# Kernel optimization log

Hardware: AMD Instinct MI355X
Metric: run time of the kernel (lower is better)

## Reference

```python
import jax, jax.numpy as jnp
import numpy as np

MODEL_DIM = 768
NUM_HEADS = 6
HEAD_DIM = 128
T = 4096
EPS = float(jnp.finfo(jnp.float32).eps)


def _rms_norm(x):
    # F.rms_norm(x, (x.size(-1),)) with no weight
    return x * jax.lax.rsqrt(jnp.mean(x * x, axis=-1, keepdims=True) + EPS)


def _rotary_tables(max_len, head_dim):
    # angular_freq: (1/1024)**linspace(0,1,dim//4) then pad dim//4 zeros -> half dim = dim//2
    nf = head_dim // 4
    af = (1.0 / 1024.0) ** jnp.linspace(0.0, 1.0, nf, dtype=jnp.float32)
    af = jnp.concatenate([af, jnp.zeros(nf, dtype=jnp.float32)])  # [head_dim//2]
    t = jnp.arange(max_len, dtype=jnp.float32)
    theta = jnp.einsum('i,j->ij', t, af)  # [max_len, head_dim//2]
    return jnp.cos(theta), jnp.sin(theta)


def _apply_rotary(x_bthd, pos_id, cos_tab, sin_tab):
    cos = cos_tab[pos_id][:, None, :]  # [T,1,hd/2] -> broadcast over heads
    sin = sin_tab[pos_id][:, None, :]
    x1, x2 = jnp.split(x_bthd.astype(jnp.float32), 2, axis=-1)
    y1 = x1 * cos + x2 * sin
    y2 = -x1 * sin + x2 * cos
    return jnp.concatenate([y1, y2], axis=-1).astype(x_bthd.dtype)


def setup_inputs() -> dict:
    key = jax.random.key(0)
    ks = jax.random.split(key, 8)
    bound = (3.0 ** 0.5) * 0.5 * MODEL_DIM ** (-0.5)  # CastedLinear init
    x = jax.random.normal(ks[0], (1, T, MODEL_DIM), dtype=jnp.float32)
    v_residual = jax.random.normal(ks[1], (1, T, NUM_HEADS, HEAD_DIM), dtype=jnp.float32)
    pos_id = jnp.arange(T, dtype=jnp.int32)
    mask = jnp.tril(jnp.ones((T, T), dtype=bool))  # causal block_mask equivalent
    Wq = jax.random.uniform(ks[2], (MODEL_DIM, MODEL_DIM), jnp.float32, -bound, bound)
    Wk = jax.random.uniform(ks[3], (MODEL_DIM, MODEL_DIM), jnp.float32, -bound, bound)
    Wv = jax.random.uniform(ks[4], (MODEL_DIM, MODEL_DIM), jnp.float32, -bound, bound)
    Wo = jax.random.uniform(ks[5], (MODEL_DIM, MODEL_DIM), jnp.float32, -bound, bound)
    lamb = jnp.float32(0.5)
    return {"x": x, "v_residual": v_residual, "Wq": Wq, "Wk": Wk, "Wv": Wv,
            "Wo": Wo, "lamb": lamb, "pos_id": pos_id, "mask": mask}


def reference(x, v_residual, Wq, Wk, Wv, Wo, lamb, pos_id, mask):
    B, Tn, _ = x.shape
    cos_tab, sin_tab = _rotary_tables(Tn, HEAD_DIM)
    # QKV projections (F.linear: x @ W.T)
    q = (x @ Wq.T).reshape(B, Tn, NUM_HEADS, HEAD_DIM)
    k = (x @ Wk.T).reshape(B, Tn, NUM_HEADS, HEAD_DIM)
    v = (x @ Wv.T).reshape(B, Tn, NUM_HEADS, HEAD_DIM)
    q = _apply_rotary(_rms_norm(q), pos_id, cos_tab, sin_tab)
    k = _apply_rotary(_rms_norm(k), pos_id, cos_tab, sin_tab)
    # value-residual mixing
    v = (1.0 - lamb) * v + lamb * v_residual
    # attention with block mask (scale = 1/sqrt(head_dim), flex_attention default)
    scale = 1.0 / (HEAD_DIM ** 0.5)
    scores = jnp.einsum('bthd,bshd->bhts', q, k) * scale  # [B,H,T,T]
    scores = jnp.where(mask[None, None, :, :], scores, -jnp.inf)
    attn = jax.nn.softmax(scores, axis=-1)
    y = jnp.einsum('bhts,bshd->bthd', attn, v).reshape(B, Tn, NUM_HEADS * HEAD_DIM)
    return (y @ Wo.T, v_residual)
```

## Files before the change

### kernel.cpp

```cpp
#include <hip/hip_runtime.h>
#include <hip/hip_bf16.h>

typedef unsigned short u16;
typedef __attribute__((ext_vector_type(8))) short short8;
typedef __attribute__((ext_vector_type(4))) float f32x4;
typedef __attribute__((ext_vector_type(16))) float f32x16;
typedef __attribute__((ext_vector_type(2))) unsigned int u32x2;

#define MODEL 768
#define SCALE2 0.1275174137f

__device__ __forceinline__ float bf2f(u16 u) {
  unsigned int x = ((unsigned int)u) << 16;
  return __uint_as_float(x);
}
__device__ __forceinline__ u16 f2bf(float f) {
  unsigned int x = __float_as_uint(f);
  unsigned int r = (x + 0x7FFFu + ((x >> 16) & 1u)) >> 16;
  return (u16)r;
}
__device__ __forceinline__ void lds_ld16(const u16* g, u16* l) {
  __builtin_amdgcn_global_load_lds((const __attribute__((address_space(1))) void*)g,
                                   (__attribute__((address_space(3))) void*)l, 16, 0, 0);
}
__device__ __forceinline__ unsigned int cvtpk_bf16(float lo, float hi_) {
  unsigned int r;
  asm("v_cvt_pk_bf16_f32 %0, %1, %2" : "=v"(r) : "v"(lo), "v"(hi_));
  return r;
}

__global__ __launch_bounds__(256) void r24_cvt(const float* __restrict__ x,
                                               const float* __restrict__ wq,
                                               const float* __restrict__ wk,
                                               const float* __restrict__ wv,
                                               u16* __restrict__ xb,
                                               u16* __restrict__ wqb,
                                               u16* __restrict__ wkb,
                                               u16* __restrict__ wvb) {
  int i = blockIdx.x * 256 + threadIdx.x;
  const float* src;
  u16* dst;
  int j;
  if (i < 786432) { src = x; dst = xb; j = i; }
  else if (i < 933888) { src = wq; dst = wqb; j = i - 786432; }
  else if (i < 1081344) { src = wk; dst = wkb; j = i - 933888; }
  else { src = wv; dst = wvb; j = i - 1081344; }
  float4 v = ((const float4*)src)[j];
  ushort4 o;
  o.x = f2bf(v.x); o.y = f2bf(v.y); o.z = f2bf(v.z); o.w = f2bf(v.w);
  ((ushort4*)dst)[j] = o;
}

__global__ __launch_bounds__(256) void r24_gemm_qkv(const u16* __restrict__ A,
                                                    const u16* __restrict__ W0,
                                                    const u16* __restrict__ W1,
                                                    const u16* __restrict__ W2,
                                                    u16* __restrict__ C0,
                                                    u16* __restrict__ C1,
                                                    u16* __restrict__ C2) {
  const u16* Wb = (blockIdx.z == 0) ? W0 : (blockIdx.z == 1) ? W1 : W2;
  u16* C = (blockIdx.z == 0) ? C0 : (blockIdx.z == 1) ? C1 : C2;
  __shared__ u16 As[64 * 64];
  __shared__ u16 Bs[128 * 64];
  const int tid = threadIdx.x;
  const int w = tid >> 6, l = tid & 63;
  const int lr = l & 15, lg = l >> 4;
  const int m0 = blockIdx.x * 64, n0 = blockIdx.y * 128;
  const int wr = (w >> 1) * 32, wc = (w & 1) * 64;
  const int srow = l >> 3;
  const int sblk = l & 7;
  f32x4 acc[2][4] = {};
  for (int k0 = 0; k0 < 768; k0 += 64) {
    __syncthreads();
#pragma unroll
    for (int i = 0; i < 2; i++) {
      int ii = w * 2 + i;
      int row = ii * 8 + srow;
      int blk = sblk ^ (row & 7);
      lds_ld16(A + (size_t)(m0 + row) * 768 + k0 + blk * 8, As + ii * 512);
    }
#pragma unroll
    for (int i = 0; i < 4; i++) {
      int ii = w * 4 + i;
      int row = ii * 8 + srow;
      int blk = sblk ^ (row & 7);
      lds_ld16(Wb + (size_t)(n0 + row) * 768 + k0 + blk * 8, Bs + ii * 512);
    }
    __syncthreads();
#pragma unroll
    for (int kk = 0; kk < 2; kk++) {
      short8 af[2], bfr[4];
#pragma unroll
      for (int mr = 0; mr < 2; mr++) {
        int r = wr + mr * 16 + lr;
        af[mr] = *(const short8*)(As + r * 64 + (((kk * 4 + lg) ^ (r & 7)) * 8));
      }
#pragma unroll
      for (int nc = 0; nc < 4; nc++) {
        int r = wc + nc * 16 + lr;
        bfr[nc] = *(const short8*)(Bs + r * 64 + (((kk * 4 + lg) ^ (r & 7)) * 8));
      }
#pragma unroll
      for (int mr = 0; mr < 2; mr++)
#pragma unroll
        for (int nc = 0; nc < 4; nc++)
          acc[mr][nc] = __builtin_amdgcn_mfma_f32_16x16x32_bf16(af[mr], bfr[nc], acc[mr][nc], 0, 0, 0);
    }
  }
#pragma unroll
  for (int mr = 0; mr < 2; mr++)
#pragma unroll
    for (int nc = 0; nc < 4; nc++)
#pragma unroll
      for (int ri = 0; ri < 4; ri++) {
        int row = m0 + wr + mr * 16 + lg * 4 + ri;
        int col = n0 + wc + nc * 16 + lr;
        C[(size_t)row * 768 + col] = f2bf(acc[mr][nc][ri]);
      }
}

__global__ __launch_bounds__(256) void r24_gemm_proj(const float* __restrict__ accO,
                                                     const float* __restrict__ accL,
                                                     const u16* __restrict__ Wb,
                                                     float* __restrict__ C) {
  __shared__ u16 As[64 * 64];
  __shared__ u16 Bs[128 * 64];
  const int tid = threadIdx.x;
  const int w = tid >> 6, l = tid & 63;
  const int lr = l & 15, lg = l >> 4;
  const int m0 = blockIdx.x * 64, n0 = blockIdx.y * 128;
  const int wr = (w >> 1) * 32, wc = (w & 1) * 64;
  const int arow = tid >> 2;
  const int ab0 = (tid & 3) * 2;
  const int srow = l >> 3;
  const int sblk = l & 7;
  f32x4 acc[2][4] = {};
  for (int k0 = 0; k0 < 768; k0 += 64) {
    __syncthreads();
    {
      const float* ap = accO + (size_t)(m0 + arow) * 768 + k0 + ab0 * 8;
      float rl = 1.0f / accL[(m0 + arow) * 6 + (k0 >> 7)];
      float4 f0 = ((const float4*)ap)[0];
      float4 f1 = ((const float4*)ap)[1];
      float4 f2 = ((const float4*)ap)[2];
      float4 f3 = ((const float4*)ap)[3];
      union { ushort4 u4[2]; short8 v; } p0, p1;
      p0.u4[0].x = f2bf(f0.x * rl); p0.u4[0].y = f2bf(f0.y * rl);
      p0.u4[0].z = f2bf(f0.z * rl); p0.u4[0].w = f2bf(f0.w * rl);
      p0.u4[1].x = f2bf(f1.x * rl); p0.u4[1].y = f2bf(f1.y * rl);
      p0.u4[1].z = f2bf(f1.z * rl); p0.u4[1].w = f2bf(f1.w * rl);
      p1.u4[0].x = f2bf(f2.x * rl); p1.u4[0].y = f2bf(f2.y * rl);
      p1.u4[0].z = f2bf(f2.z * rl); p1.u4[0].w = f2bf(f2.w * rl);
      p1.u4[1].x = f2bf(f3.x * rl); p1.u4[1].y = f2bf(f3.y * rl);
      p1.u4[1].z = f2bf(f3.z * rl); p1.u4[1].w = f2bf(f3.w * rl);
      *(short8*)(As + arow * 64 + ((ab0 ^ (arow & 7)) * 8)) = p0.v;
      *(short8*)(As + arow * 64 + (((ab0 + 1) ^ (arow & 7)) * 8)) = p1.v;
    }
#pragma unroll
    for (int i = 0; i < 4; i++) {
      int ii = w * 4 + i;
      int row = ii * 8 + srow;
      int blk = sblk ^ (row & 7);
      lds_ld16(Wb + (size_t)(n0 + row) * 768 + k0 + blk * 8, Bs + ii * 512);
    }
    __syncthreads();
#pragma unroll
    for (int kk = 0; kk < 2; kk++) {
      short8 af[2], bfr[4];
#pragma unroll
      for (int mr = 0; mr < 2; mr++) {
        int r = wr + mr * 16 + lr;
        af[mr] = *(const short8*)(As + r * 64 + (((kk * 4 + lg) ^ (r & 7)) * 8));
      }
#pragma unroll
      for (int nc = 0; nc < 4; nc++) {
        int r = wc + nc * 16 + lr;
        bfr[nc] = *(const short8*)(Bs + r * 64 + (((kk * 4 + lg) ^ (r & 7)) * 8));
      }
#pragma unroll
      for (int mr = 0; mr < 2; mr++)
#pragma unroll
        for (int nc = 0; nc < 4; nc++)
          acc[mr][nc] = __builtin_amdgcn_mfma_f32_16x16x32_bf16(af[mr], bfr[nc], acc[mr][nc], 0, 0, 0);
    }
  }
#pragma unroll
  for (int mr = 0; mr < 2; mr++)
#pragma unroll
    for (int nc = 0; nc < 4; nc++)
#pragma unroll
      for (int ri = 0; ri < 4; ri++) {
        int row = m0 + wr + mr * 16 + lg * 4 + ri;
        int col = n0 + wc + nc * 16 + lr;
        C[(size_t)row * 768 + col] = acc[mr][nc][ri];
      }
}

__global__ __launch_bounds__(256) void r24_normrope(u16* __restrict__ qb,
                                                    u16* __restrict__ kb,
                                                    u16* __restrict__ vb,
                                                    const float* __restrict__ vres,
                                                    const float* __restrict__ lambp,
                                                    const int* __restrict__ pos,
                                                    float* __restrict__ out1,
                                                    float* __restrict__ accZ,
                                                    const float* __restrict__ wo,
                                                    u16* __restrict__ wob) {
  {
    int gid = blockIdx.x * 256 + threadIdx.x;
    if (gid < 792576) {
      float4 z = {0.0f, 0.0f, 0.0f, 0.0f};
      ((float4*)accZ)[gid] = z;
    } else if (gid < 792576 + 147456) {
      int j = gid - 792576;
      float4 v = ((const float4*)wo)[j];
      ushort4 o;
      o.x = f2bf(v.x); o.y = f2bf(v.y); o.z = f2bf(v.z); o.w = f2bf(v.w);
      ((ushort4*)wob)[j] = o;
    }
  }
  const int wg = blockIdx.x * 4 + (threadIdx.x >> 6);
  const int l = threadIdx.x & 63;
  const int t = wg / 6;
  const int h = wg - t * 6;
  const size_t base = (size_t)t * MODEL + h * 128;
  const float EPS = 1.1920928955078125e-07f;

  float c = 1.0f, sn = 0.0f;
  if (l < 32) {
    float af = exp2f(-10.0f * (float)l * (1.0f / 31.0f));
    float th = (float)pos[t] * af;
    sincosf(th, &sn, &c);
  }
  {
    float a = bf2f(qb[base + l]), b = bf2f(qb[base + 64 + l]);
    float ss = a * a + b * b;
#pragma unroll
    for (int off = 32; off; off >>= 1) ss += __shfl_xor(ss, off);
    float r = rsqrtf(ss * (1.0f / 128.0f) + EPS) * SCALE2;
    float an = a * r, bn = b * r;
    qb[base + l] = f2bf(an * c + bn * sn);
    qb[base + 64 + l] = f2bf(bn * c - an * sn);
  }
  {
    float a = bf2f(kb[base + l]), b = bf2f(kb[base + 64 + l]);
    float ss = a * a + b * b;
#pragma unroll
    for (int off = 32; off; off >>= 1) ss += __shfl_xor(ss, off);
    float r = rsqrtf(ss * (1.0f / 128.0f) + EPS);
    float an = a * r, bn = b * r;
    kb[base + l] = f2bf(an * c + bn * sn);
    kb[base + 64 + l] = f2bf(bn * c - an * sn);
  }
  {
    float lm = *lambp;
    float a = bf2f(vb[base + l]), b = bf2f(vb[base + 64 + l]);
    float ra = vres[base + l], rb = vres[base + 64 + l];
    vb[base + l] = f2bf((1.0f - lm) * a + lm * ra);
    vb[base + 64 + l] = f2bf((1.0f - lm) * b + lm * rb);
    out1[base + l] = ra;
    out1[base + 64 + l] = rb;
  }
}

__global__ __launch_bounds__(256, 2) void r24_attn(const u16* __restrict__ Q,
                                                   const u16* __restrict__ K,
                                                   const u16* __restrict__ V,
                                                   float* __restrict__ accO,
                                                   float* __restrict__ accL) {
  const int bx = blockIdx.x;
  const int h = bx / 80;
  const int u = 79 - (bx - h * 80);
  int qt, kc;
  if (u < 8)       { qt = u;                      kc = 0; }
  else if (u < 24) { int v = u - 8;  qt = 8 + (v >> 1); kc = v & 1; }
  else if (u < 48) { int v = u - 24; int q3 = v / 3; qt = 16 + q3; kc = v - 3 * q3; }
  else             { int v = u - 48; qt = 24 + (v >> 2); kc = v & 3; }
  const int rowmax = 128 * qt + 127;
  const int c0 = kc << 10;
  const bool islast = (c0 + 1024 > rowmax);
  const int cend = islast ? (rowmax + 1) : (c0 + 1024);
  const int niter = (cend - c0 + 63) >> 6;

  const int tid = threadIdx.x;
  const int wv = tid >> 6, l = tid & 63;
  const int lq = l & 31;
  const int hi = l >> 5;

  __shared__ u16 Ks[64][128];
  __shared__ u16 vt[128][72];

  const int c_ = tid & 31, cc = c_ * 4, g = tid >> 5;
  const int vswz = (c_ & 7) << 3;

  const int qr = qt * 128 + wv * 32;
  const int qrow = qr + lq;

  short8 ones;
#pragma unroll
  for (int i = 0; i < 8; i++) ones[i] = (short)0x3F80;

  short8 qf[8];
  {
    const u16* qp = Q + (size_t)qrow * 768 + h * 128 + hi * 8;
#pragma unroll
    for (int s = 0; s < 8; s++) qf[s] = *(const short8*)(qp + s * 16);
  }
  f32x16 oacc[4] = {};
  f32x16 lacc = {};

  for (int kv = 0; kv < niter; kv++) {
    const int k0 = c0 + kv * 64;

#pragma unroll
    for (int i = 0; i < 4; i++) {
      int rbase = wv * 16 + i * 4;
      int row = rbase + (l >> 4);
      int blk = (l & 15) ^ (row & 7);
      lds_ld16(K + (size_t)(k0 + row) * 768 + h * 128 + blk * 8, &Ks[rbase][0]);
    }
#pragma unroll
    for (int it = 0; it < 2; it++) {
      int quad = g + 8 * it;
      int r0 = 4 * quad;
      const u16* vp = V + (size_t)(k0 + r0) * 768 + h * 128 + cc;
      ushort4 v0 = *(const ushort4*)(vp);
      ushort4 v1 = *(const ushort4*)(vp + 768);
      ushort4 v2 = *(const ushort4*)(vp + 1536);
      ushort4 v3 = *(const ushort4*)(vp + 2304);
      int rs4 = r0 ^ vswz;
      ushort4 t4;
      t4.x = v0.x; t4.y = v1.x; t4.z = v2.x; t4.w = v3.x;
      *(ushort4*)&vt[cc + 0][rs4] = t4;
      t4.x = v0.y; t4.y = v1.y; t4.z = v2.y; t4.w = v3.y;
      *(ushort4*)&vt[cc + 1][rs4] = t4;
      t4.x = v0.z; t4.y = v1.z; t4.z = v2.z; t4.w = v3.z;
      *(ushort4*)&vt[cc + 2][rs4] = t4;
      t4.x = v0.w; t4.y = v1.w; t4.z = v2.w; t4.w = v3.w;
      *(ushort4*)&vt[cc + 3][rs4] = t4;
    }
    __syncthreads();

    f32x16 sac0 = {}, sac1 = {};
    __builtin_amdgcn_s_setprio(1);
    {
      const int r0_ = lq, r1_ = 32 + lq;
#pragma unroll
      for (int s = 0; s < 8; s++) {
        short8 kf0 = *(const short8*)(&Ks[r0_][((s * 2 + hi) ^ (r0_ & 7)) * 8]);
        sac0 = __builtin_amdgcn_mfma_f32_32x32x16_bf16(kf0, qf[s], sac0, 0, 0, 0);
      }
#pragma unroll
      for (int s = 0; s < 8; s++) {
        short8 kf1 = *(const short8*)(&Ks[r1_][((s * 2 + hi) ^ (r1_ & 7)) * 8]);
        sac1 = __builtin_amdgcn_mfma_f32_32x32x16_bf16(kf1, qf[s], sac1, 0, 0, 0);
      }
    }
    __builtin_amdgcn_s_setprio(0);

    float p[32];
    const bool maskit = islast && (k0 + 63 > qr);
    if (maskit) {
#pragma unroll
      for (int r = 0; r < 16; r++) {
        int kvg = k0 + (r & 3) + 8 * (r >> 2) + 4 * hi;
        p[r] = (kvg <= qrow) ? exp2f(sac0[r]) : 0.0f;
      }
#pragma unroll
      for (int r = 0; r < 16; r++) {
        int kvg = k0 + 32 + (r & 3) + 8 * (r >> 2) + 4 * hi;
        p[16 + r] = (kvg <= qrow) ? exp2f(sac1[r]) : 0.0f;
      }
    } else {
#pragma unroll
      for (int r = 0; r < 16; r++) p[r] = exp2f(sac0[r]);
#pragma unroll
      for (int r = 0; r < 16; r++) p[16 + r] = exp2f(sac1[r]);
    }

    union { unsigned int w[4]; short8 v; } pa[4];
#pragma unroll
    for (int s = 0; s < 4; s++) {
      const int b = s * 8;
      unsigned int cA0 = cvtpk_bf16(p[b + 0], p[b + 1]);
      unsigned int cA1 = cvtpk_bf16(p[b + 2], p[b + 3]);
      unsigned int cB0 = cvtpk_bf16(p[b + 4], p[b + 5]);
      unsigned int cB1 = cvtpk_bf16(p[b + 6], p[b + 7]);
      u32x2 s0 = __builtin_amdgcn_permlane32_swap(cA0, cB0, false, false);
      u32x2 s1 = __builtin_amdgcn_permlane32_swap(cA1, cB1, false, false);
      pa[s].w[0] = s0[0]; pa[s].w[1] = s1[0]; pa[s].w[2] = s0[1]; pa[s].w[3] = s1[1];
    }

    __builtin_amdgcn_s_setprio(1);
#pragma unroll
    for (int s = 0; s < 4; s++)
      lacc = __builtin_amdgcn_mfma_f32_32x32x16_bf16(pa[s].v, ones, lacc, 0, 0, 0);
#pragma unroll
    for (int dt = 0; dt < 4; dt++) {
      const int d = dt * 32 + lq;
      const int dz = ((d >> 2) & 7) << 3;
#pragma unroll
      for (int s = 0; s < 4; s++) {
        short8 vf = *(const short8*)(&vt[d][(s * 16 + hi * 8) ^ dz]);
        oacc[dt] = __builtin_amdgcn_mfma_f32_32x32x16_bf16(pa[s].v, vf, oacc[dt], 0, 0, 0);
      }
    }
    __builtin_amdgcn_s_setprio(0);
    __syncthreads();
  }

#pragma unroll
  for (int dt = 0; dt < 4; dt++) {
    const int d = dt * 32 + lq;
#pragma unroll
    for (int r = 0; r < 16; r++) {
      int qrw = qr + (r & 3) + 8 * (r >> 2) + 4 * hi;
      unsafeAtomicAdd(&accO[(size_t)qrw * 768 + h * 128 + d], oacc[dt][r]);
    }
  }
  if (lq == 0) {
#pragma unroll
    for (int r = 0; r < 16; r++) {
      int qrw = qr + (r & 3) + 8 * (r >> 2) + 4 * hi;
      unsafeAtomicAdd(&accL[qrw * 6 + h], lacc[r]);
    }
  }
}

extern "C" void kernel_launch(void* const* d_in, const int* in_sizes, int n_in,
                              void* d_out, int out_size, void* d_ws, size_t ws_size,
                              hipStream_t stream) {
  const float* x = (const float*)d_in[0];
  const float* vres = (const float*)d_in[1];
  const float* Wq = (const float*)d_in[2];
  const float* Wk = (const float*)d_in[3];
  const float* Wv = (const float*)d_in[4];
  const float* Wo = (const float*)d_in[5];
  const float* lamb = (const float*)d_in[6];
  const int* pos = (const int*)d_in[7];
  float* out = (float*)d_out;

  u16* xb = (u16*)d_ws;
  u16* qb = xb + 3145728;
  u16* kb = qb + 3145728;
  u16* vb = kb + 3145728;
  float* accO = (float*)((char*)d_ws + 25165824);
  float* accL = accO + 3145728;
  u16* wqb = (u16*)accO;
  u16* wkb = wqb + 589824;
  u16* wvb = wkb + 589824;
  u16* wob = xb;
  float* out1 = out + 3145728;

  r24_cvt<<<4800, 256, 0, stream>>>(x, Wq, Wk, Wv, xb, wqb, wkb, wvb);
  r24_gemm_qkv<<<dim3(64, 6, 3), 256, 0, stream>>>(xb, wqb, wkb, wvb, qb, kb, vb);
  r24_normrope<<<6144, 256, 0, stream>>>(qb, kb, vb, vres, lamb, pos, out1,
                                         accO, Wo, wob);
  r24_attn<<<480, 256, 0, stream>>>(qb, kb, vb, accO, accL);
  r24_gemm_proj<<<dim3(64, 6), 256, 0, stream>>>(accO, accL, wob, out);
}
```

Baseline: 129.7 us.

## Double-buffer K/V tiles in attention to overlap next-tile loads with compute

Result: faster. 126.1 us (-2.7%).

```diff
diff --git a/kernel.cpp b/kernel.cpp
--- a/kernel.cpp
+++ b/kernel.cpp
@@ -29,7 +29,7 @@
   return r;
 }
 
-__global__ __launch_bounds__(256) void r24_cvt(const float* __restrict__ x,
+__global__ __launch_bounds__(256) void r25_cvt(const float* __restrict__ x,
                                                const float* __restrict__ wq,
                                                const float* __restrict__ wk,
                                                const float* __restrict__ wv,
@@ -51,7 +51,7 @@
   ((ushort4*)dst)[j] = o;
 }
 
-__global__ __launch_bounds__(256) void r24_gemm_qkv(const u16* __restrict__ A,
+__global__ __launch_bounds__(256) void r25_gemm_qkv(const u16* __restrict__ A,
                                                     const u16* __restrict__ W0,
                                                     const u16* __restrict__ W1,
                                                     const u16* __restrict__ W2,
@@ -119,7 +119,7 @@
       }
 }
 
-__global__ __launch_bounds__(256) void r24_gemm_proj(const float* __restrict__ accO,
+__global__ __launch_bounds__(256) void r25_gemm_proj(const float* __restrict__ accO,
                                                      const float* __restrict__ accL,
                                                      const u16* __restrict__ Wb,
                                                      float* __restrict__ C) {
@@ -196,7 +196,7 @@
       }
 }
 
-__global__ __launch_bounds__(256) void r24_normrope(u16* __restrict__ qb,
+__global__ __launch_bounds__(256) void r25_normrope(u16* __restrict__ qb,
                                                     u16* __restrict__ kb,
                                                     u16* __restrict__ vb,
                                                     const float* __restrict__ vres,
@@ -263,7 +263,7 @@
   }
 }
 
-__global__ __launch_bounds__(256, 2) void r24_attn(const u16* __restrict__ Q,
+__global__ __launch_bounds__(256, 2) void r25_attn(const u16* __restrict__ Q,
                                                    const u16* __restrict__ K,
                                                    const u16* __restrict__ V,
                                                    float* __restrict__ accO,
@@ -287,8 +287,8 @@
   const int lq = l & 31;
   const int hi = l >> 5;
 
-  __shared__ u16 Ks[64][128];
-  __shared__ u16 vt[128][72];
+  __shared__ u16 Ks[2][64][128];
+  __shared__ u16 vt[2][128][72];
 
   const int c_ = tid & 31, cc = c_ * 4, g = tid >> 5;
   const int vswz = (c_ & 7) << 3;
@@ -309,37 +309,60 @@
   f32x16 oacc[4] = {};
   f32x16 lacc = {};
 
+#pragma unroll
+  for (int i = 0; i < 4; i++) {
+    int rbase = wv * 16 + i * 4;
+    int row = rbase + (l >> 4);
+    int blk = (l & 15) ^ (row & 7);
+    lds_ld16(K + (size_t)(c0 + row) * 768 + h * 128 + blk * 8, &Ks[0][rbase][0]);
+  }
+#pragma unroll
+  for (int it = 0; it < 2; it++) {
+    int quad = g + 8 * it;
+    int r0 = 4 * quad;
+    const u16* vp = V + (size_t)(c0 + r0) * 768 + h * 128 + cc;
+    ushort4 v0 = *(const ushort4*)(vp);
+    ushort4 v1 = *(const ushort4*)(vp + 768);
+    ushort4 v2 = *(const ushort4*)(vp + 1536);
+    ushort4 v3 = *(const ushort4*)(vp + 2304);
+    int rs4 = r0 ^ vswz;
+    ushort4 t4;
+    t4.x = v0.x; t4.y = v1.x; t4.z = v2.x; t4.w = v3.x;
+    *(ushort4*)&vt[0][cc + 0][rs4] = t4;
+    t4.x = v0.y; t4.y = v1.y; t4.z = v2.y; t4.w = v3.y;
+    *(ushort4*)&vt[0][cc + 1][rs4] = t4;
+    t4.x = v0.z; t4.y = v1.z; t4.z = v2.z; t4.w = v3.z;
+    *(ushort4*)&vt[0][cc + 2][rs4] = t4;
+    t4.x = v0.w; t4.y = v1.w; t4.z = v2.w; t4.w = v3.w;
+    *(ushort4*)&vt[0][cc + 3][rs4] = t4;
+  }
+  __syncthreads();
+
   for (int kv = 0; kv < niter; kv++) {
+    const int cur = kv & 1, nxt = cur ^ 1;
     const int k0 = c0 + kv * 64;
-
-#pragma unroll
-    for (int i = 0; i < 4; i++) {
-      int rbase = wv * 16 + i * 4;
-      int row = rbase + (l >> 4);
-      int blk = (l & 15) ^ (row & 7);
-      lds_ld16(K + (size_t)(k0 + row) * 768 + h * 128 + blk * 8, &Ks[rbase][0]);
-    }
-#pragma unroll
-    for (int it = 0; it < 2; it++) {
-      int quad = g + 8 * it;
-      int r0 = 4 * quad;
-      const u16* vp = V + (size_t)(k0 + r0) * 768 + h * 128 + cc;
-      ushort4 v0 = *(const ushort4*)(vp);
-      ushort4 v1 = *(const ushort4*)(vp + 768);
-      ushort4 v2 = *(const ushort4*)(vp + 1536);
-      ushort4 v3 = *(const ushort4*)(vp + 2304);
-      int rs4 = r0 ^ vswz;
-      ushort4 t4;
-      t4.x = v0.x; t4.y = v1.x; t4.z = v2.x; t4.w = v3.x;
-      *(ushort4*)&vt[cc + 0][rs4] = t4;
-      t4.x = v0.y; t4.y = v1.y; t4.z = v2.y; t4.w = v3.y;
-      *(ushort4*)&vt[cc + 1][rs4] = t4;
-      t4.x = v0.z; t4.y = v1.z; t4.z = v2.z; t4.w = v3.z;
-      *(ushort4*)&vt[cc + 2][rs4] = t4;
-      t4.x = v0.w; t4.y = v1.w; t4.z = v2.w; t4.w = v3.w;
-      *(ushort4*)&vt[cc + 3][rs4] = t4;
-    }
-    __syncthreads();
+    const bool pre = (kv + 1 < niter);
+
+    ushort4 vr[2][4];
+    if (pre) {
+      const int k0n = k0 + 64;
+#pragma unroll
+      for (int i = 0; i < 4; i++) {
+        int rbase = wv * 16 + i * 4;
+        int row = rbase + (l >> 4);
+        int blk = (l & 15) ^ (row & 7);
+        lds_ld16(K + (size_t)(k0n + row) * 768 + h * 128 + blk * 8, &Ks[nxt][rbase][0]);
+      }
+#pragma unroll
+      for (int it = 0; it < 2; it++) {
+        int r0 = 4 * (g + 8 * it);
+        const u16* vp = V + (size_t)(k0n + r0) * 768 + h * 128 + cc;
+        vr[it][0] = *(const ushort4*)(vp);
+        vr[it][1] = *(const ushort4*)(vp + 768);
+        vr[it][2] = *(const ushort4*)(vp + 1536);
+        vr[it][3] = *(const ushort4*)(vp + 2304);
+      }
+    }
 
     f32x16 sac0 = {}, sac1 = {};
     __builtin_amdgcn_s_setprio(1);
@@ -347,12 +370,12 @@
       const int r0_ = lq, r1_ = 32 + lq;
 #pragma unroll
       for (int s = 0; s < 8; s++) {
-        short8 kf0 = *(const short8*)(&Ks[r0_][((s * 2 + hi) ^ (r0_ & 7)) * 8]);
+        short8 kf0 = *(const short8*)(&Ks[cur][r0_][((s * 2 + hi) ^ (r0_ & 7)) * 8]);
         sac0 = __builtin_amdgcn_mfma_f32_32x32x16_bf16(kf0, qf[s], sac0, 0, 0, 0);
       }
 #pragma unroll
       for (int s = 0; s < 8; s++) {
-        short8 kf1 = *(const short8*)(&Ks[r1_][((s * 2 + hi) ^ (r1_ & 7)) * 8]);
+        short8 kf1 = *(const short8*)(&Ks[cur][r1_][((s * 2 + hi) ^ (r1_ & 7)) * 8]);
         sac1 = __builtin_amdgcn_mfma_f32_32x32x16_bf16(kf1, qf[s], sac1, 0, 0, 0);
       }
     }
@@ -401,11 +424,28 @@
       const int dz = ((d >> 2) & 7) << 3;
 #pragma unroll
       for (int s = 0; s < 4; s++) {
-        short8 vf = *(const short8*)(&vt[d][(s * 16 + hi * 8) ^ dz]);
+        short8 vf = *(const short8*)(&vt[cur][d][(s * 16 + hi * 8) ^ dz]);
         oacc[dt] = __builtin_amdgcn_mfma_f32_32x32x16_bf16(pa[s].v, vf, oacc[dt], 0, 0, 0);
       }
     }
     __builtin_amdgcn_s_setprio(0);
+
+    if (pre) {
+#pragma unroll
+      for (int it = 0; it < 2; it++) {
+        int r0 = 4 * (g + 8 * it);
+        int rs4 = r0 ^ vswz;
+        ushort4 t4;
+        t4.x = vr[it][0].x; t4.y = vr[it][1].x; t4.z = vr[it][2].x; t4.w = vr[it][3].x;
+        *(ushort4*)&vt[nxt][cc + 0][rs4] = t4;
+        t4.x = vr[it][0].y; t4.y = vr[it][1].y; t4.z = vr[it][2].y; t4.w = vr[it][3].y;
+        *(ushort4*)&vt[nxt][cc + 1][rs4] = t4;
+        t4.x = vr[it][0].z; t4.y = vr[it][1].z; t4.z = vr[it][2].z; t4.w = vr[it][3].z;
+        *(ushort4*)&vt[nxt][cc + 2][rs4] = t4;
+        t4.x = vr[it][0].w; t4.y = vr[it][1].w; t4.z = vr[it][2].w; t4.w = vr[it][3].w;
+        *(ushort4*)&vt[nxt][cc + 3][rs4] = t4;
+      }
+    }
     __syncthreads();
   }
 
@@ -452,10 +492,10 @@
   u16* wob = xb;
   float* out1 = out + 3145728;
 
-  r24_cvt<<<4800, 256, 0, stream>>>(x, Wq, Wk, Wv, xb, wqb, wkb, wvb);
-  r24_gemm_qkv<<<dim3(64, 6, 3), 256, 0, stream>>>(xb, wqb, wkb, wvb, qb, kb, vb);
-  r24_normrope<<<6144, 256, 0, stream>>>(qb, kb, vb, vres, lamb, pos, out1,
+  r25_cvt<<<4800, 256, 0, stream>>>(x, Wq, Wk, Wv, xb, wqb, wkb, wvb);
+  r25_gemm_qkv<<<dim3(64, 6, 3), 256, 0, stream>>>(xb, wqb, wkb, wvb, qb, kb, vb);
+  r25_normrope<<<6144, 256, 0, stream>>>(qb, kb, vb, vres, lamb, pos, out1,
                                          accO, Wo, wob);
-  r24_attn<<<480, 256, 0, stream>>>(qb, kb, vb, accO, accL);
-  r24_gemm_proj<<<dim3(64, 6), 256, 0, stream>>>(accO, accL, wob, out);
-}
+  r25_attn<<<480, 256, 0, stream>>>(qb, kb, vb, accO, accL);
+  r25_gemm_proj<<<dim3(64, 6), 256, 0, stream>>>(accO, accL, wob, out);
+}
```
